# Performance work log

Measured on AMD Instinct MI355X. Metric: run time of the kernel, lower is better.

Reference implementation:

```python
import jax, jax.numpy as jnp
import numpy as np

B, T = 256, 512
LATENT, COND, HID, OUT = 128, 32, 512, 64
IN_DIM = OUT + COND  # LSTM input dim = output_dim + condition_dim


def setup_inputs() -> dict:
    key = jax.random.key(0)
    ks = jax.random.split(key, 14)
    def lin(k, fan_in, shape):
        return jax.random.uniform(k, shape, jnp.float32, -1.0, 1.0) / np.sqrt(fan_in)
    return {
        "latent_vector": jax.random.normal(ks[0], (B, LATENT), jnp.float32),
        "conditions": jax.random.normal(ks[1], (B, COND), jnp.float32),
        "target_sequences": jax.random.normal(ks[2], (B, T, OUT), jnp.float32),
        # latent_to_hidden / latent_to_cell
        "W_lh": lin(ks[3], LATENT, (HID, LATENT)), "b_lh": lin(ks[4], LATENT, (HID,)),
        "W_lc": lin(ks[5], LATENT, (HID, LATENT)), "b_lc": lin(ks[6], LATENT, (HID,)),
        # LSTM weights, torch gate order [i, f, g, o]
        "W_ih": lin(ks[7], HID, (4 * HID, IN_DIM)), "W_hh": lin(ks[8], HID, (4 * HID, HID)),
        "b_ih": lin(ks[9], HID, (4 * HID,)), "b_hh": lin(ks[10], HID, (4 * HID,)),
        # hidden_to_output
        "W_out": lin(ks[11], HID, (OUT, HID)), "b_out": lin(ks[12], HID, (OUT,)),
        "output_lengths": jnp.full((B,), T, dtype=jnp.int32),
    }


def _decode(latent_vector, conditions, target_sequences,
            W_lh, b_lh, W_lc, b_lc, W_ih, W_hh, b_ih, b_hh, W_out, b_out):
    Bb = latent_vector.shape[0]
    Tm = target_sequences.shape[1]  # == output_lengths.max(), static under jit
    D = target_sequences.shape[-1]
    h0 = latent_vector @ W_lh.T + b_lh  # (B, H)
    c0 = latent_vector @ W_lc.T + b_lc  # (B, H)
    init = jnp.ones((Bb, 1, D), target_sequences.dtype)  # initial SOH = 1
    # Teacher forcing (sampling_probability=1.0): step t (t=1..Tm-1) consumes
    # ones at t=1, target[:, t-1] afterwards -> inputs known upfront.
    prev = jnp.concatenate([init, target_sequences[:, 1:Tm - 1, :]], axis=1)  # (B, Tm-1, D)
    cond = jnp.broadcast_to(conditions[:, None, :], (Bb, Tm - 1, conditions.shape[-1]))
    xs = jnp.concatenate([prev, cond], axis=-1)  # (B, Tm-1, D+C)
    # Precompute input contribution to gates for all steps (one big GEMM).
    gx = jnp.einsum('btd,gd->tbg', xs, W_ih) + (b_ih + b_hh)  # (Tm-1, B, 4H)

    def step(carry, g_t):
        h, c = carry
        g = g_t + h @ W_hh.T
        i, f, gg, o = jnp.split(g, 4, axis=-1)
        c = jax.nn.sigmoid(f) * c + jax.nn.sigmoid(i) * jnp.tanh(gg)
        h = jax.nn.sigmoid(o) * jnp.tanh(c)
        return (h, c), h

    _, hs = jax.lax.scan(step, (h0, c0), gx)  # hs: (Tm-1, B, H)
    preds = jnp.einsum('tbh,dh->btd', hs, W_out) + b_out  # (B, Tm-1, D)
    return jnp.concatenate([init, preds], axis=1)  # (B, Tm, D)


def reference(latent_vector, conditions, target_sequences,
              W_lh, b_lh, W_lc, b_lc, W_ih, W_hh, b_ih, b_hh, W_out, b_out,
              output_lengths):
    # output_lengths are all == T; max length is static for jit.
    return _decode(latent_vector, conditions, target_sequences,
                   W_lh, b_lh, W_lc, b_lc, W_ih, W_hh, b_ih, b_hh, W_out, b_out)
```

## Files before the change

kernel.cpp:

```cpp
#include <hip/hip_runtime.h>

#define Bx    256
#define Tx    512
#define LAT   128
#define CND   32
#define HIDN  512
#define OUTD  64
#define KD    608
#define KP    616
#define ROWS  32
#define NCOLS 32

typedef unsigned short u16;
typedef unsigned int   u32;
typedef short s16x8 __attribute__((ext_vector_type(8)));
typedef unsigned short u16x8 __attribute__((ext_vector_type(8)));
typedef unsigned short u16x4 __attribute__((ext_vector_type(4)));
typedef float f32x4 __attribute__((ext_vector_type(4)));

#define WG_SLICE (NCOLS * KP * 2)
#define WG_OFF   0
#define WG_BYTES (64 * WG_SLICE)
#define H0_OFF   (WG_BYTES)
#define H1_OFF   (H0_OFF + Bx * HIDN * 2)
#define CB_OFF   (H1_OFF + Bx * HIDN * 2)
#define BS_OFF   (CB_OFF + Bx * HIDN * 4)
#define DN_OFF   (BS_OFF + 4 * HIDN * 4)

#define A_BYTES  (ROWS * KP * 2)
#define SMEM_SZ  (2 * A_BYTES + HIDN * 4)
#define WCHUNK   (A_BYTES / 16)

__device__ __forceinline__ float sigmoidf_(float x) { return 1.0f / (1.0f + __expf(-x)); }

__device__ __forceinline__ u16 f2bf(float f) {
    union { float f; u32 u; } v; v.f = f;
    u32 r = (v.u + 0x7FFFu + ((v.u >> 16) & 1u)) >> 16;
    return (u16)r;
}
__device__ __forceinline__ float bf2f(u16 s) {
    union { u32 u; float f; } v; v.u = ((u32)s) << 16;
    return v.f;
}
__device__ __forceinline__ void gl_lds16(const void* g, void* l) {
    __builtin_amdgcn_global_load_lds(
        (const __attribute__((address_space(1))) unsigned int*)g,
        (__attribute__((address_space(3))) unsigned int*)l, 16, 0, 0);
}
__device__ __forceinline__ u32 agent_ld(const u32* p) {
    return __hip_atomic_load(p, __ATOMIC_RELAXED, __HIP_MEMORY_SCOPE_AGENT);
}
__device__ __forceinline__ void agent_st(u32* p, u32 v) {
    __hip_atomic_store(p, v, __ATOMIC_RELAXED, __HIP_MEMORY_SCOPE_AGENT);
}

__global__ __launch_bounds__(256) void prep_w(
    const float* __restrict__ W_ih, const float* __restrict__ W_hh,
    const float* __restrict__ b_ih, const float* __restrict__ b_hh,
    u16* __restrict__ Wg, float* __restrict__ bsum, u32* __restrict__ done_arr)
{
    const int idx = blockIdx.x * 256 + threadIdx.x;
    if (idx < 64 * NCOLS * KD) {
        const int k   = idx % KD;
        const int t   = idx / KD;
        const int col = t % NCOLS;
        const int hs  = t / NCOLS;
        const int g = col >> 3, u = col & 7;
        const int n = g * HIDN + hs * 8 + u;
        const float v = (k < 96) ? W_ih[n * 96 + k] : W_hh[n * HIDN + (k - 96)];
        Wg[(hs * NCOLS + col) * KP + k] = f2bf(v);
    }
    if (idx < 4 * HIDN) bsum[idx] = b_ih[idx] + b_hh[idx];
    if (idx < 8 * 64)   done_arr[idx] = 0u;
}

__global__ __launch_bounds__(256) void init_kernel(
    const float* __restrict__ latent, const float* __restrict__ W_lh,
    const float* __restrict__ b_lh,   const float* __restrict__ W_lc,
    const float* __restrict__ b_lc,   u16* __restrict__ h0,
    float* __restrict__ c0,           float* __restrict__ out)
{
    const int b = blockIdx.x;
    const float4* lat4 = reinterpret_cast<const float4*>(latent + b * LAT);
#pragma unroll
    for (int jj = 0; jj < 2; ++jj) {
        const int j = threadIdx.x + jj * 256;
        const float4* wh4 = reinterpret_cast<const float4*>(W_lh + j * LAT);
        const float4* wc4 = reinterpret_cast<const float4*>(W_lc + j * LAT);
        float sh = 0.f, sc = 0.f;
#pragma unroll 8
        for (int k = 0; k < LAT / 4; ++k) {
            float4 l = lat4[k], a = wh4[k], c = wc4[k];
            sh += l.x * a.x + l.y * a.y + l.z * a.z + l.w * a.w;
            sc += l.x * c.x + l.y * c.y + l.z * c.z + l.w * c.w;
        }
        h0[b * HIDN + j] = f2bf(sh + b_lh[j]);
        c0[b * HIDN + j] = sc + b_lc[j];
    }
    if (threadIdx.x < OUTD) out[b * (Tx * OUTD) + threadIdx.x] = 1.0f;
}

__global__ __launch_bounds__(256, 2) void persist_kernel(
    const float* __restrict__ target, const float* __restrict__ cond,
    u16* __restrict__ hbuf0, u16* __restrict__ hbuf1,
    const float* __restrict__ cbuf, const u16* __restrict__ Wg,
    const float* __restrict__ bsum, const float* __restrict__ W_out,
    const float* __restrict__ b_out, float* __restrict__ out,
    u32* __restrict__ done)
{
    const int tid  = threadIdx.x;
    const int bs   = blockIdx.x & 7;
    const int hs   = blockIdx.x >> 3;
    const int w    = tid >> 6;
    const int lane = tid & 63;

    __shared__ __align__(16) char smem[SMEM_SZ];
    u16*   As   = (u16*)smem;
    u16*   Ws   = (u16*)(smem + A_BYTES);
    float* Wo   = (float*)(smem + 2 * A_BYTES);
    float* gbuf = (float*)smem;

    {
        const u16* wsrc = Wg + hs * (NCOLS * KP);
#pragma unroll
        for (int it = 0; it < 10; ++it) {
            const int base = it * 256 + w * 64;
            if (base + lane < WCHUNK)
                gl_lds16(wsrc + (base + lane) * 8, (void*)(Ws + base * 8));
        }
    }
    if (tid < 128)
        reinterpret_cast<float4*>(Wo)[tid] =
            reinterpret_cast<const float4*>(W_out + hs * HIDN)[tid];

    const int r_  = tid >> 3, q_ = tid & 7;
    const int gb_ = bs * ROWS + r_;
    const int hu_ = hs * 8 + q_;
    float c_reg = cbuf[gb_ * HIDN + hu_];
    const float bsum0 = bsum[0 * HIDN + hu_];
    const float bsum1 = bsum[1 * HIDN + hu_];
    const float bsum2 = bsum[2 * HIDN + hu_];
    const float bsum3 = bsum[3 * HIDN + hu_];
    const float bo    = b_out[hs];

    u16x4 cond_bf;
    {
        const float4 cv = *reinterpret_cast<const float4*>(cond + gb_ * CND + q_ * 4);
        cond_bf[0] = f2bf(cv.x); cond_bf[1] = f2bf(cv.y);
        cond_bf[2] = f2bf(cv.z); cond_bf[3] = f2bf(cv.w);
    }

    const int mrow = ((w & 1) << 4) + (lane & 15);
    const int ncol = ((w >> 1) << 4) + (lane & 15);
    const int kq   = (lane >> 4) << 3;
    const u16* ap  = As + mrow * KP + kq;
    const u16* bp  = Ws + ncol * KP + kq;
    const int row0 = ((w & 1) << 4) + ((lane >> 4) << 2);

    for (int j = 0; j < Tx; ++j) {
        if (j < Tx - 1) {
            u16x8 xv;
            if (j == 0) {
#pragma unroll
                for (int m = 0; m < 8; ++m) xv[m] = 0x3F80;
            } else {
                const float* tg = target + (gb_ * Tx + j) * OUTD + q_ * 8;
                const float4 t0 = *reinterpret_cast<const float4*>(tg);
                const float4 t1 = *reinterpret_cast<const float4*>(tg + 4);
                xv[0]=f2bf(t0.x); xv[1]=f2bf(t0.y); xv[2]=f2bf(t0.z); xv[3]=f2bf(t0.w);
                xv[4]=f2bf(t1.x); xv[5]=f2bf(t1.y); xv[6]=f2bf(t1.z); xv[7]=f2bf(t1.w);
            }
            *reinterpret_cast<u16x8*>(As + r_ * KP + q_ * 8)      = xv;
            *reinterpret_cast<u16x4*>(As + r_ * KP + 64 + q_ * 4) = cond_bf;
        }

        if (j > 0 && tid < 64) {
            const u32* fp = done + bs * 64 + tid;
            for (;;) {
                u32 v = agent_ld(fp);
                if (__all((int)(v >= (u32)j))) break;
            }
        }
        __syncthreads();

        {
            const u16* hp = (j & 1) ? hbuf1 : hbuf0;
            const u32* hp32 = (const u32*)(hp + bs * ROWS * HIDN);
            u32 hv[32];
#pragma unroll
            for (int i = 0; i < 32; ++i)
                hv[i] = agent_ld(hp32 + i * 256 + tid);
#pragma unroll
            for (int i = 0; i < 32; ++i)
                *(((u32*)(As + i * KP + 96)) + tid) = hv[i];
        }
        __syncthreads();

        if (j >= 1) {
            const u16*   hrow = As + r_ * KP + 96 + q_ * 64;
            const float* wo   = Wo + q_ * 64;
            float p = 0.f;
#pragma unroll
            for (int i = 0; i < 8; ++i) {
                const int ii = (i + q_) & 7;
                u16x8 hv  = *reinterpret_cast<const u16x8*>(hrow + ii * 8);
                float4 w0 = *reinterpret_cast<const float4*>(wo + ii * 8);
                float4 w1 = *reinterpret_cast<const float4*>(wo + ii * 8 + 4);
                p += bf2f(hv[0])*w0.x + bf2f(hv[1])*w0.y + bf2f(hv[2])*w0.z + bf2f(hv[3])*w0.w
                   + bf2f(hv[4])*w1.x + bf2f(hv[5])*w1.y + bf2f(hv[6])*w1.z + bf2f(hv[7])*w1.w;
            }
            p += __shfl_xor(p, 1); p += __shfl_xor(p, 2); p += __shfl_xor(p, 4);
            if (q_ == 0) out[gb_ * (Tx * OUTD) + j * OUTD + hs] = p + bo;
        }
        if (j == Tx - 1) break;

        f32x4 acc = {0.f, 0.f, 0.f, 0.f};
#pragma unroll
        for (int ck = 0; ck < 19; ++ck) {
            s16x8 a = *reinterpret_cast<const s16x8*>(ap + ck * 32);
            s16x8 b = *reinterpret_cast<const s16x8*>(bp + ck * 32);
            acc = __builtin_amdgcn_mfma_f32_16x16x32_bf16(a, b, acc, 0, 0, 0);
        }
        __syncthreads();
#pragma unroll
        for (int t = 0; t < 4; ++t) gbuf[(row0 + t) * 36 + ncol] = acc[t];
        __syncthreads();

        {
            const float gi = gbuf[r_ * 36 +      q_] + bsum0;
            const float gf = gbuf[r_ * 36 +  8 + q_] + bsum1;
            const float gg = gbuf[r_ * 36 + 16 + q_] + bsum2;
            const float go = gbuf[r_ * 36 + 24 + q_] + bsum3;
            const float ig = sigmoidf_(gi), fg = sigmoidf_(gf);
            const float gt = tanhf(gg),     og = sigmoidf_(go);
            c_reg = fg * c_reg + ig * gt;
            const u32 hb = (u32)f2bf(og * tanhf(c_reg));
            const u32 nb = (u32)__shfl_xor((int)hb, 1);
            if ((q_ & 1) == 0) {
                u16* hn = (j & 1) ? hbuf0 : hbuf1;
                agent_st(((u32*)(hn + gb_ * HIDN)) + (hu_ >> 1), hb | (nb << 16));
            }
        }
        asm volatile("s_waitcnt vmcnt(0)" ::: "memory");
        __syncthreads();
        if (tid == 0)
            agent_st(done + bs * 64 + hs, (u32)(j + 1));
    }
}

__global__ __launch_bounds__(256, 2) void step_kernel(
    int j,
    const float* __restrict__ target, const float* __restrict__ cond,
    const u16* __restrict__ hprev,    u16* __restrict__ hnext,
    float* __restrict__ cbuf,         const u16* __restrict__ Wg,
    const float* __restrict__ bsum,
    const float* __restrict__ W_out,  const float* __restrict__ b_out,
    float* __restrict__ out)
{
    const int tid  = threadIdx.x;
    const int bs   = blockIdx.x >> 6;
    const int hs   = blockIdx.x & 63;
    const int w    = tid >> 6;
    const int lane = tid & 63;

    if (j >= 1) {
        const int r = tid >> 3, q = tid & 7;
        const int gb = bs * ROWS + r;
        const u16*   hp = hprev + gb * HIDN + q * 64;
        const float* wo = W_out + hs * HIDN + q * 64;
        float p = 0.f;
#pragma unroll
        for (int i = 0; i < 8; ++i) {
            u16x8 hv = *reinterpret_cast<const u16x8*>(hp + i * 8);
            float4 w0 = *reinterpret_cast<const float4*>(wo + i * 8);
            float4 w1 = *reinterpret_cast<const float4*>(wo + i * 8 + 4);
            p += bf2f(hv[0]) * w0.x + bf2f(hv[1]) * w0.y + bf2f(hv[2]) * w0.z + bf2f(hv[3]) * w0.w
               + bf2f(hv[4]) * w1.x + bf2f(hv[5]) * w1.y + bf2f(hv[6]) * w1.z + bf2f(hv[7]) * w1.w;
        }
        p += __shfl_xor(p, 1); p += __shfl_xor(p, 2); p += __shfl_xor(p, 4);
        if (q == 0) out[gb * (Tx * OUTD) + j * OUTD + hs] = p + b_out[hs];
    }
    if (j >= Tx - 1) return;

    __shared__ __align__(16) char smem[2 * ROWS * KP * 2 + 1536];
    u16*   As   = (u16*)smem;
    u16*   Ws   = (u16*)(smem + ROWS * KP * 2);
    float* gbuf = (float*)smem;

    {
        const int r = tid >> 3, t8 = tid & 7;
        const int gb = bs * ROWS + r;
        const float* tg = target + (gb * Tx + j) * OUTD;
#pragma unroll
        for (int m = 0; m < 12; ++m) {
            const int k = t8 * 12 + m;
            float v;
            if (k < OUTD) v = (j == 0) ? 1.0f : tg[k];
            else          v = cond[gb * CND + (k - OUTD)];
            As[r * KP + k] = f2bf(v);
        }
    }
#pragma unroll
    for (int it = 0; it < 8; ++it) {
        const int rr = w + it * 4;
        gl_lds16(hprev + (bs * ROWS + rr) * HIDN + lane * 8, (void*)(As + rr * KP + 96));
    }
    {
        const u16* wsrc = Wg + hs * (NCOLS * KP);
#pragma unroll
        for (int it = 0; it < 10; ++it) {
            const int seg = it * 256 + w * 64;
            gl_lds16(wsrc + seg * 8 + lane * 8, (void*)(Ws + seg * 8));
        }
    }
    __syncthreads();

    const int mrow = ((w & 1) << 4) + (lane & 15);
    const int ncol = ((w >> 1) << 4) + (lane & 15);
    const int kq   = (lane >> 4) << 3;
    const u16* ap = As + mrow * KP + kq;
    const u16* bp = Ws + ncol * KP + kq;
    f32x4 acc = {0.f, 0.f, 0.f, 0.f};
#pragma unroll
    for (int ck = 0; ck < 19; ++ck) {
        s16x8 a = *reinterpret_cast<const s16x8*>(ap + ck * 32);
        s16x8 b = *reinterpret_cast<const s16x8*>(bp + ck * 32);
        acc = __builtin_amdgcn_mfma_f32_16x16x32_bf16(a, b, acc, 0, 0, 0);
    }
    __syncthreads();

    {
        const int row0 = ((w & 1) << 4) + ((lane >> 4) << 2);
#pragma unroll
        for (int t = 0; t < 4; ++t) gbuf[(row0 + t) * 36 + ncol] = acc[t];
    }
    __syncthreads();

    {
        const int r = tid >> 3, u = tid & 7;
        const int gb = bs * ROWS + r, hu = hs * 8 + u;
        const float gi = gbuf[r * 36 +      u] + bsum[0 * HIDN + hu];
        const float gf = gbuf[r * 36 +  8 + u] + bsum[1 * HIDN + hu];
        const float gg = gbuf[r * 36 + 16 + u] + bsum[2 * HIDN + hu];
        const float go = gbuf[r * 36 + 24 + u] + bsum[3 * HIDN + hu];
        const float ig = sigmoidf_(gi), fg = sigmoidf_(gf);
        const float gt = tanhf(gg),     og = sigmoidf_(go);
        const float co = cbuf[gb * HIDN + hu];
        const float cn = fg * co + ig * gt;
        cbuf[gb * HIDN + hu]  = cn;
        hnext[gb * HIDN + hu] = f2bf(og * tanhf(cn));
    }
}

extern "C" void kernel_launch(void* const* d_in, const int* in_sizes, int n_in,
                              void* d_out, int out_size, void* d_ws, size_t ws_size,
                              hipStream_t stream) {
    const float* latent = (const float*)d_in[0];
    const float* cond   = (const float*)d_in[1];
    const float* target = (const float*)d_in[2];
    const float* W_lh   = (const float*)d_in[3];
    const float* b_lh   = (const float*)d_in[4];
    const float* W_lc   = (const float*)d_in[5];
    const float* b_lc   = (const float*)d_in[6];
    const float* W_ih   = (const float*)d_in[7];
    const float* W_hh   = (const float*)d_in[8];
    const float* b_ih   = (const float*)d_in[9];
    const float* b_hh   = (const float*)d_in[10];
    const float* W_out  = (const float*)d_in[11];
    const float* b_out  = (const float*)d_in[12];

    float* out = (float*)d_out;
    char*  ws  = (char*)d_ws;
    u16*   Wg    = (u16*)(ws + WG_OFF);
    u16*   hbuf0 = (u16*)(ws + H0_OFF);
    u16*   hbuf1 = (u16*)(ws + H1_OFF);
    float* cbuf  = (float*)(ws + CB_OFF);
    float* bsum  = (float*)(ws + BS_OFF);
    u32*   done  = (u32*)(ws + DN_OFF);

    hipLaunchKernelGGL(prep_w, dim3(4864), dim3(256), 0, stream,
                       W_ih, W_hh, b_ih, b_hh, Wg, bsum, done);
    hipLaunchKernelGGL(init_kernel, dim3(Bx), dim3(256), 0, stream,
                       latent, W_lh, b_lh, W_lc, b_lc, hbuf0, cbuf, out);

    {
        const float* t_  = target;  const float* c_  = cond;
        u16*         h0_ = hbuf0;   u16*         h1_ = hbuf1;
        const float* cb_ = cbuf;    const u16*   wg_ = Wg;
        const float* bs_ = bsum;    const float* wo_ = W_out;
        const float* bo_ = b_out;   float*       o_  = out;
        u32*         dn_ = done;
        void* args[] = { &t_, &c_, &h0_, &h1_, &cb_, &wg_, &bs_, &wo_, &bo_, &o_, &dn_ };
        hipError_t err = hipLaunchCooperativeKernel(
            reinterpret_cast<const void*>(persist_kernel),
            dim3(512), dim3(256), args, 0, stream);
        if (err != hipSuccess) {
            for (int j = 0; j < Tx; ++j) {
                u16* hp = (j & 1) ? hbuf1 : hbuf0;
                u16* hn = (j & 1) ? hbuf0 : hbuf1;
                hipLaunchKernelGGL(step_kernel, dim3(512), dim3(256), 0, stream,
                                   j, target, cond, hp, hn, cbuf,
                                   Wg, bsum, W_out, b_out, out);
            }
        }
    }
}
```

Baseline: 2.456 ms.

## Replace done-flag barrier with tagged 64-bit hidden-state words for per-element sync

Removes the separate per-block done counters and the vmcnt drain plus flag store after each step. Each hidden-state pair is now written as a 64-bit word that carries an epoch/step tag. Consumers poll their own words until the tags match, so data and readiness travel in one store. This cuts one global round trip and a barrier per timestep. In exchange it doubles the hidden-state traffic, adds polling loops, and relies on an epoch counter in the workspace persisting across calls.

```diff
diff --git a/kernel.cpp b/kernel.cpp
--- a/kernel.cpp
+++ b/kernel.cpp
@@ -13,6 +13,7 @@
 
 typedef unsigned short u16;
 typedef unsigned int   u32;
+typedef unsigned long long u64;
 typedef short s16x8 __attribute__((ext_vector_type(8)));
 typedef unsigned short u16x8 __attribute__((ext_vector_type(8)));
 typedef unsigned short u16x4 __attribute__((ext_vector_type(4)));
@@ -25,7 +26,8 @@
 #define H1_OFF   (H0_OFF + Bx * HIDN * 2)
 #define CB_OFF   (H1_OFF + Bx * HIDN * 2)
 #define BS_OFF   (CB_OFF + Bx * HIDN * 4)
-#define DN_OFF   (BS_OFF + 4 * HIDN * 4)
+#define HT_OFF   (BS_OFF + 4 * HIDN * 4)
+#define EP_OFF   (HT_OFF + 2 * Bx * 256 * 8)
 
 #define A_BYTES  (ROWS * KP * 2)
 #define SMEM_SZ  (2 * A_BYTES + HIDN * 4)
@@ -47,17 +49,17 @@
         (const __attribute__((address_space(1))) unsigned int*)g,
         (__attribute__((address_space(3))) unsigned int*)l, 16, 0, 0);
 }
-__device__ __forceinline__ u32 agent_ld(const u32* p) {
+__device__ __forceinline__ u64 agent_ld64(const u64* p) {
     return __hip_atomic_load(p, __ATOMIC_RELAXED, __HIP_MEMORY_SCOPE_AGENT);
 }
-__device__ __forceinline__ void agent_st(u32* p, u32 v) {
+__device__ __forceinline__ void agent_st64(u64* p, u64 v) {
     __hip_atomic_store(p, v, __ATOMIC_RELAXED, __HIP_MEMORY_SCOPE_AGENT);
 }
 
 __global__ __launch_bounds__(256) void prep_w(
     const float* __restrict__ W_ih, const float* __restrict__ W_hh,
     const float* __restrict__ b_ih, const float* __restrict__ b_hh,
-    u16* __restrict__ Wg, float* __restrict__ bsum, u32* __restrict__ done_arr)
+    u16* __restrict__ Wg, float* __restrict__ bsum, u32* __restrict__ epoch)
 {
     const int idx = blockIdx.x * 256 + threadIdx.x;
     if (idx < 64 * NCOLS * KD) {
@@ -71,17 +73,20 @@
         Wg[(hs * NCOLS + col) * KP + k] = f2bf(v);
     }
     if (idx < 4 * HIDN) bsum[idx] = b_ih[idx] + b_hh[idx];
-    if (idx < 8 * 64)   done_arr[idx] = 0u;
+    if (blockIdx.x == 0 && threadIdx.x == 0) *epoch = *epoch + 1u;
 }
 
 __global__ __launch_bounds__(256) void init_kernel(
     const float* __restrict__ latent, const float* __restrict__ W_lh,
     const float* __restrict__ b_lh,   const float* __restrict__ W_lc,
     const float* __restrict__ b_lc,   u16* __restrict__ h0,
-    float* __restrict__ c0,           float* __restrict__ out)
+    float* __restrict__ c0,           float* __restrict__ out,
+    u64* __restrict__ ht,             const u32* __restrict__ epoch)
 {
     const int b = blockIdx.x;
+    const u32 tag0 = (*epoch) << 9;
     const float4* lat4 = reinterpret_cast<const float4*>(latent + b * LAT);
+    u32 hbits[2];
 #pragma unroll
     for (int jj = 0; jj < 2; ++jj) {
         const int j = threadIdx.x + jj * 256;
@@ -94,25 +99,34 @@
             sh += l.x * a.x + l.y * a.y + l.z * a.z + l.w * a.w;
             sc += l.x * c.x + l.y * c.y + l.z * c.z + l.w * c.w;
         }
-        h0[b * HIDN + j] = f2bf(sh + b_lh[j]);
+        const u16 hb = f2bf(sh + b_lh[j]);
+        hbits[jj] = (u32)hb;
+        h0[b * HIDN + j] = hb;
         c0[b * HIDN + j] = sc + b_lc[j];
+    }
+    const u32 n0 = (u32)__shfl_xor((int)hbits[0], 1);
+    const u32 n1 = (u32)__shfl_xor((int)hbits[1], 1);
+    if (!(threadIdx.x & 1)) {
+        const int half = threadIdx.x >> 1;
+        ht[b * 256 + half]       = (((u64)tag0) << 32) | (hbits[0] | (n0 << 16));
+        ht[b * 256 + 128 + half] = (((u64)tag0) << 32) | (hbits[1] | (n1 << 16));
     }
     if (threadIdx.x < OUTD) out[b * (Tx * OUTD) + threadIdx.x] = 1.0f;
 }
 
 __global__ __launch_bounds__(256, 2) void persist_kernel(
     const float* __restrict__ target, const float* __restrict__ cond,
-    u16* __restrict__ hbuf0, u16* __restrict__ hbuf1,
-    const float* __restrict__ cbuf, const u16* __restrict__ Wg,
-    const float* __restrict__ bsum, const float* __restrict__ W_out,
-    const float* __restrict__ b_out, float* __restrict__ out,
-    u32* __restrict__ done)
+    u64* __restrict__ ht,             const float* __restrict__ cbuf,
+    const u16* __restrict__ Wg,       const float* __restrict__ bsum,
+    const float* __restrict__ W_out,  const float* __restrict__ b_out,
+    float* __restrict__ out,          const u32* __restrict__ epoch)
 {
     const int tid  = threadIdx.x;
     const int bs   = blockIdx.x & 7;
     const int hs   = blockIdx.x >> 3;
     const int w    = tid >> 6;
     const int lane = tid & 63;
+    const u32 tbase = (*epoch) << 9;
 
     __shared__ __align__(16) char smem[SMEM_SZ];
     u16*   As   = (u16*)smem;
@@ -174,27 +188,33 @@
             *reinterpret_cast<u16x4*>(As + r_ * KP + 64 + q_ * 4) = cond_bf;
         }
 
-        if (j > 0 && tid < 64) {
-            const u32* fp = done + bs * 64 + tid;
-            for (;;) {
-                u32 v = agent_ld(fp);
-                if (__all((int)(v >= (u32)j))) break;
-            }
-        }
-        __syncthreads();
-
         {
-            const u16* hp = (j & 1) ? hbuf1 : hbuf0;
-            const u32* hp32 = (const u32*)(hp + bs * ROWS * HIDN);
-            u32 hv[32];
-#pragma unroll
-            for (int i = 0; i < 32; ++i)
-                hv[i] = agent_ld(hp32 + i * 256 + tid);
-#pragma unroll
-            for (int i = 0; i < 32; ++i)
-                *(((u32*)(As + i * KP + 96)) + tid) = hv[i];
-        }
-        __syncthreads();
+            const u64* hp64 = ht + (size_t)(j & 1) * (Bx * 256) + (bs * ROWS) * 256 + tid;
+            const u32  texp = tbase + (u32)j;
+            u32 need = 0xFFFFFFFFu;
+            u64 v[32];
+#pragma unroll
+            for (int i = 0; i < 32; ++i) v[i] = agent_ld64(hp64 + i * 256);
+#pragma unroll
+            for (int i = 0; i < 32; ++i) {
+                if ((u32)(v[i] >> 32) == texp) {
+                    need &= ~(1u << i);
+                    *(((u32*)(As + i * KP + 96)) + tid) = (u32)v[i];
+                }
+            }
+            while (!__syncthreads_and((int)(need == 0u))) {
+#pragma unroll
+                for (int i = 0; i < 32; ++i) {
+                    if (need & (1u << i)) {
+                        u64 vv = agent_ld64(hp64 + i * 256);
+                        if ((u32)(vv >> 32) == texp) {
+                            need &= ~(1u << i);
+                            *(((u32*)(As + i * KP + 96)) + tid) = (u32)vv;
+                        }
+                    }
+                }
+            }
+        }
 
         if (j >= 1) {
             const u16*   hrow = As + r_ * KP + 96 + q_ * 64;
@@ -236,15 +256,13 @@
             c_reg = fg * c_reg + ig * gt;
             const u32 hb = (u32)f2bf(og * tanhf(c_reg));
             const u32 nb = (u32)__shfl_xor((int)hb, 1);
-            if ((q_ & 1) == 0) {
-                u16* hn = (j & 1) ? hbuf0 : hbuf1;
-                agent_st(((u32*)(hn + gb_ * HIDN)) + (hu_ >> 1), hb | (nb << 16));
-            }
-        }
-        asm volatile("s_waitcnt vmcnt(0)" ::: "memory");
+            if (!(q_ & 1)) {
+                u64* hn = ht + (size_t)((j + 1) & 1) * (Bx * 256);
+                agent_st64(hn + gb_ * 256 + (hu_ >> 1),
+                           (((u64)(tbase + (u32)(j + 1))) << 32) | (hb | (nb << 16)));
+            }
+        }
         __syncthreads();
-        if (tid == 0)
-            agent_st(done + bs * 64 + hs, (u32)(j + 1));
     }
 }
 
@@ -376,21 +394,21 @@
     u16*   hbuf1 = (u16*)(ws + H1_OFF);
     float* cbuf  = (float*)(ws + CB_OFF);
     float* bsum  = (float*)(ws + BS_OFF);
-    u32*   done  = (u32*)(ws + DN_OFF);
+    u64*   ht    = (u64*)(ws + HT_OFF);
+    u32*   epoch = (u32*)(ws + EP_OFF);
 
     hipLaunchKernelGGL(prep_w, dim3(4864), dim3(256), 0, stream,
-                       W_ih, W_hh, b_ih, b_hh, Wg, bsum, done);
+                       W_ih, W_hh, b_ih, b_hh, Wg, bsum, epoch);
     hipLaunchKernelGGL(init_kernel, dim3(Bx), dim3(256), 0, stream,
-                       latent, W_lh, b_lh, W_lc, b_lc, hbuf0, cbuf, out);
+                       latent, W_lh, b_lh, W_lc, b_lc, hbuf0, cbuf, out, ht, epoch);
 
     {
         const float* t_  = target;  const float* c_  = cond;
-        u16*         h0_ = hbuf0;   u16*         h1_ = hbuf1;
-        const float* cb_ = cbuf;    const u16*   wg_ = Wg;
-        const float* bs_ = bsum;    const float* wo_ = W_out;
-        const float* bo_ = b_out;   float*       o_  = out;
-        u32*         dn_ = done;
-        void* args[] = { &t_, &c_, &h0_, &h1_, &cb_, &wg_, &bs_, &wo_, &bo_, &o_, &dn_ };
+        u64*         ht_ = ht;      const float* cb_ = cbuf;
+        const u16*   wg_ = Wg;      const float* bs_ = bsum;
+        const float* wo_ = W_out;   const float* bo_ = b_out;
+        float*       o_  = out;     const u32*   ep_ = epoch;
+        void* args[] = { &t_, &c_, &ht_, &cb_, &wg_, &bs_, &wo_, &bo_, &o_, &ep_ };
         hipError_t err = hipLaunchCooperativeKernel(
             reinterpret_cast<const void*>(persist_kernel),
             dim3(512), dim3(256), args, 0, stream);
```

New measurement: 6.244 ms. +154.3%, slower.

## Use per-wave done flags and 64-bit h exchange, defer output projection past signal

Applied to the files above, without the earlier changes.

The persistent LSTM kernel now has each wave publish its own completion flag, so the block-wide barrier before signalling is gone. Consumers poll pairs of flags with 64-bit loads, and every thread waits only on the flags covering the hidden-state columns it reads. This merges the flag wait and the h load into one phase with a single barrier. Hidden states are packed four bf16 per 64-bit store/load, and the gate scratch rows are padded to a new stride. The output projection for step j now runs after the done signal, overlapping it with other blocks' progress. The tradeoffs are four times as many flags and more polling traffic, plus reliance on relaxed-ordering correctness per wave.

```diff
diff --git a/kernel.cpp b/kernel.cpp
--- a/kernel.cpp
+++ b/kernel.cpp
@@ -13,6 +13,7 @@
 
 typedef unsigned short u16;
 typedef unsigned int   u32;
+typedef unsigned long long u64;
 typedef short s16x8 __attribute__((ext_vector_type(8)));
 typedef unsigned short u16x8 __attribute__((ext_vector_type(8)));
 typedef unsigned short u16x4 __attribute__((ext_vector_type(4)));
@@ -30,6 +31,7 @@
 #define A_BYTES  (ROWS * KP * 2)
 #define SMEM_SZ  (2 * A_BYTES + HIDN * 4)
 #define WCHUNK   (A_BYTES / 16)
+#define RB       1232
 
 __device__ __forceinline__ float sigmoidf_(float x) { return 1.0f / (1.0f + __expf(-x)); }
 
@@ -51,6 +53,12 @@
     return __hip_atomic_load(p, __ATOMIC_RELAXED, __HIP_MEMORY_SCOPE_AGENT);
 }
 __device__ __forceinline__ void agent_st(u32* p, u32 v) {
+    __hip_atomic_store(p, v, __ATOMIC_RELAXED, __HIP_MEMORY_SCOPE_AGENT);
+}
+__device__ __forceinline__ u64 agent_ld64(const u64* p) {
+    return __hip_atomic_load(p, __ATOMIC_RELAXED, __HIP_MEMORY_SCOPE_AGENT);
+}
+__device__ __forceinline__ void agent_st64(u64* p, u64 v) {
     __hip_atomic_store(p, v, __ATOMIC_RELAXED, __HIP_MEMORY_SCOPE_AGENT);
 }
 
@@ -70,8 +78,8 @@
         const float v = (k < 96) ? W_ih[n * 96 + k] : W_hh[n * HIDN + (k - 96)];
         Wg[(hs * NCOLS + col) * KP + k] = f2bf(v);
     }
-    if (idx < 4 * HIDN) bsum[idx] = b_ih[idx] + b_hh[idx];
-    if (idx < 8 * 64)   done_arr[idx] = 0u;
+    if (idx < 4 * HIDN)  bsum[idx] = b_ih[idx] + b_hh[idx];
+    if (idx < 8 * 64 * 4) done_arr[idx] = 0u;
 }
 
 __global__ __launch_bounds__(256) void init_kernel(
@@ -115,10 +123,9 @@
     const int lane = tid & 63;
 
     __shared__ __align__(16) char smem[SMEM_SZ];
-    u16*   As   = (u16*)smem;
-    u16*   Ws   = (u16*)(smem + A_BYTES);
-    float* Wo   = (float*)(smem + 2 * A_BYTES);
-    float* gbuf = (float*)smem;
+    u16*   As = (u16*)smem;
+    u16*   Ws = (u16*)(smem + A_BYTES);
+    float* Wo = (float*)(smem + 2 * A_BYTES);
 
     {
         const u16* wsrc = Wg + hs * (NCOLS * KP);
@@ -149,6 +156,10 @@
         cond_bf[0] = f2bf(cv.x); cond_bf[1] = f2bf(cv.y);
         cond_bf[2] = f2bf(cv.z); cond_bf[3] = f2bf(cv.w);
     }
+
+    const int c2 = tid & 127;
+    const int rh = tid >> 7;
+    const u64* fpp = (const u64*)(done + ((bs * 64 + (c2 >> 1)) << 2) + (rh << 1));
 
     const int mrow = ((w & 1) << 4) + (lane & 15);
     const int ncol = ((w >> 1) << 4) + (lane & 15);
@@ -174,29 +185,24 @@
             *reinterpret_cast<u16x4*>(As + r_ * KP + 64 + q_ * 4) = cond_bf;
         }
 
-        if (j > 0 && tid < 64) {
-            const u32* fp = done + bs * 64 + tid;
-            for (;;) {
-                u32 v = agent_ld(fp);
-                if (__all((int)(v >= (u32)j))) break;
-            }
+        {
+            const u32 jj = (u32)j;
+            u64 f = agent_ld64(fpp);
+            while ((u32)f < jj || (u32)(f >> 32) < jj) f = agent_ld64(fpp);
+        }
+        {
+            const u64* hb = (const u64*)((j & 1) ? hbuf1 : hbuf0);
+            const u64* hp = hb + (size_t)(bs * ROWS + rh * 16) * 128 + c2;
+            u64 v[16];
+#pragma unroll
+            for (int m = 0; m < 16; ++m) v[m] = agent_ld64(hp + (size_t)m * 128);
+#pragma unroll
+            for (int m = 0; m < 16; ++m)
+                *reinterpret_cast<u64*>(As + (rh * 16 + m) * KP + 96 + c2 * 4) = v[m];
         }
         __syncthreads();
 
-        {
-            const u16* hp = (j & 1) ? hbuf1 : hbuf0;
-            const u32* hp32 = (const u32*)(hp + bs * ROWS * HIDN);
-            u32 hv[32];
-#pragma unroll
-            for (int i = 0; i < 32; ++i)
-                hv[i] = agent_ld(hp32 + i * 256 + tid);
-#pragma unroll
-            for (int i = 0; i < 32; ++i)
-                *(((u32*)(As + i * KP + 96)) + tid) = hv[i];
-        }
-        __syncthreads();
-
-        if (j >= 1) {
+        if (j == Tx - 1) {
             const u16*   hrow = As + r_ * KP + 96 + q_ * 64;
             const float* wo   = Wo + q_ * 64;
             float p = 0.f;
@@ -211,8 +217,8 @@
             }
             p += __shfl_xor(p, 1); p += __shfl_xor(p, 2); p += __shfl_xor(p, 4);
             if (q_ == 0) out[gb_ * (Tx * OUTD) + j * OUTD + hs] = p + bo;
-        }
-        if (j == Tx - 1) break;
+            break;
+        }
 
         f32x4 acc = {0.f, 0.f, 0.f, 0.f};
 #pragma unroll
@@ -223,28 +229,49 @@
         }
         __syncthreads();
 #pragma unroll
-        for (int t = 0; t < 4; ++t) gbuf[(row0 + t) * 36 + ncol] = acc[t];
+        for (int t = 0; t < 4; ++t)
+            reinterpret_cast<float*>(smem + (size_t)(row0 + t) * RB)[ncol] = acc[t];
         __syncthreads();
 
         {
-            const float gi = gbuf[r_ * 36 +      q_] + bsum0;
-            const float gf = gbuf[r_ * 36 +  8 + q_] + bsum1;
-            const float gg = gbuf[r_ * 36 + 16 + q_] + bsum2;
-            const float go = gbuf[r_ * 36 + 24 + q_] + bsum3;
+            const float* gr = reinterpret_cast<const float*>(smem + (size_t)r_ * RB);
+            const float gi = gr[     q_] + bsum0;
+            const float gf = gr[ 8 + q_] + bsum1;
+            const float gg = gr[16 + q_] + bsum2;
+            const float go = gr[24 + q_] + bsum3;
             const float ig = sigmoidf_(gi), fg = sigmoidf_(gf);
             const float gt = tanhf(gg),     og = sigmoidf_(go);
             c_reg = fg * c_reg + ig * gt;
-            const u32 hb = (u32)f2bf(og * tanhf(c_reg));
-            const u32 nb = (u32)__shfl_xor((int)hb, 1);
-            if ((q_ & 1) == 0) {
-                u16* hn = (j & 1) ? hbuf0 : hbuf1;
-                agent_st(((u32*)(hn + gb_ * HIDN)) + (hu_ >> 1), hb | (nb << 16));
+            const u32 hbit = (u32)f2bf(og * tanhf(c_reg));
+            const u32 pair = hbit | ((u32)__shfl_xor((int)hbit, 1) << 16);
+            const u64 quad = (u64)pair |
+                             ((u64)(u32)__shfl_xor((int)pair, 2) << 32);
+            if ((q_ & 3) == 0) {
+                u64* hn = (u64*)((j & 1) ? hbuf0 : hbuf1);
+                agent_st64(hn + (size_t)gb_ * 128 + hs * 2 + (q_ >> 2), quad);
             }
         }
         asm volatile("s_waitcnt vmcnt(0)" ::: "memory");
+        if (lane == 0)
+            agent_st(done + ((bs * 64 + hs) << 2) + w, (u32)(j + 1));
+
+        if (j >= 1) {
+            const u16*   hrow = As + r_ * KP + 96 + q_ * 64;
+            const float* wo   = Wo + q_ * 64;
+            float p = 0.f;
+#pragma unroll
+            for (int i = 0; i < 8; ++i) {
+                const int ii = (i + q_) & 7;
+                u16x8 hv  = *reinterpret_cast<const u16x8*>(hrow + ii * 8);
+                float4 w0 = *reinterpret_cast<const float4*>(wo + ii * 8);
+                float4 w1 = *reinterpret_cast<const float4*>(wo + ii * 8 + 4);
+                p += bf2f(hv[0])*w0.x + bf2f(hv[1])*w0.y + bf2f(hv[2])*w0.z + bf2f(hv[3])*w0.w
+                   + bf2f(hv[4])*w1.x + bf2f(hv[5])*w1.y + bf2f(hv[6])*w1.z + bf2f(hv[7])*w1.w;
+            }
+            p += __shfl_xor(p, 1); p += __shfl_xor(p, 2); p += __shfl_xor(p, 4);
+            if (q_ == 0) out[gb_ * (Tx * OUTD) + j * OUTD + hs] = p + bo;
+        }
         __syncthreads();
-        if (tid == 0)
-            agent_st(done + bs * 64 + hs, (u32)(j + 1));
     }
 }
 
```

Measured after the change: 2.314 ms. 5.8% less time.
